# Performance work log

Hardware: AMD Instinct MI355X
Metric: run time of the kernel (lower is better)

## Reference

```python
import jax, jax.numpy as jnp
import numpy as np

D_MODEL = 512
N_HEADS = 8
D_FF = 2048

def _linear_params(key, d_in, d_out):
    kw, kb = jax.random.split(key)
    bound = 1.0 / np.sqrt(d_in)
    W = jax.random.uniform(kw, (d_in, d_out), minval=-bound, maxval=bound, dtype=jnp.float32)
    b = jax.random.uniform(kb, (d_out,), minval=-bound, maxval=bound, dtype=jnp.float32)
    return W, b

def setup_inputs() -> dict:
    key = jax.random.key(0)
    ks = jax.random.split(key, 7)
    x = jax.random.normal(ks[0], (4, 2048, D_MODEL), dtype=jnp.float32)
    Wq, bq = _linear_params(ks[1], D_MODEL, D_MODEL)
    Wk, bk = _linear_params(ks[2], D_MODEL, D_MODEL)
    Wv, bv = _linear_params(ks[3], D_MODEL, D_MODEL)
    W1, b1 = _linear_params(ks[4], D_MODEL, D_FF)
    W2, b2 = _linear_params(ks[5], D_FF, D_MODEL)
    g1 = jnp.ones((D_MODEL,), jnp.float32); be1 = jnp.zeros((D_MODEL,), jnp.float32)
    g2 = jnp.ones((D_MODEL,), jnp.float32); be2 = jnp.zeros((D_MODEL,), jnp.float32)
    return {"x": x, "Wq": Wq, "bq": bq, "Wk": Wk, "bk": bk, "Wv": Wv, "bv": bv,
            "W1": W1, "b1": b1, "W2": W2, "b2": b2,
            "g1": g1, "be1": be1, "g2": g2, "be2": be2}

def _layernorm(x, g, b, eps=1e-5):
    mu = jnp.mean(x, axis=-1, keepdims=True)
    var = jnp.mean(jnp.square(x - mu), axis=-1, keepdims=True)
    return (x - mu) * jax.lax.rsqrt(var + eps) * g + b

def reference(x, Wq, bq, Wk, bk, Wv, bv, W1, b1, W2, b2, g1, be1, g2, be2):
    B, S, D = x.shape
    H = N_HEADS
    Dh = D // H
    residual = x
    xn = _layernorm(x, g1, be1)
    # [B,S,D] -> [B,H,S,Dh]
    q = (xn @ Wq + bq).reshape(B, S, H, Dh).transpose(0, 2, 1, 3)
    k = (xn @ Wk + bk).reshape(B, S, H, Dh).transpose(0, 2, 1, 3)
    v = (xn @ Wv + bv).reshape(B, S, H, Dh).transpose(0, 2, 1, 3)
    # sigmoid pointwise attention, scaled by sqrt(d_model) (not head dim)
    scores = jnp.einsum('bhsd,bhtd->bhst', q, k) / jnp.sqrt(jnp.float32(D))
    attn = jax.nn.sigmoid(scores)
    out = jnp.einsum('bhst,bhtd->bhsd', attn, v)
    out = out.transpose(0, 2, 1, 3).reshape(B, S, D)
    x = residual + out  # dropout=0 (eval)
    residual = x
    xn = _layernorm(x, g2, be2)
    ffn = jax.nn.relu(xn @ W1 + b1) @ W2 + b2
    return residual + ffn
```

## Files before the change

kernel.cpp:

```cpp
#include <hip/hip_runtime.h>
#include <hip/hip_bf16.h>
#include <math.h>

#define D_MODEL 512
#define N_HEADS 8
#define D_HEAD 64
#define D_FF 2048
#define SEQ 2048
#define BATCH 4
#define NTOK (BATCH * SEQ)
#define QSCALE 0.04419417382415922f
#define QSCALE_L2E (-QSCALE * 1.44269504089f)

typedef unsigned short ushort_t;
typedef __attribute__((ext_vector_type(8))) short short8;
typedef __attribute__((ext_vector_type(4))) short short4v;
typedef __attribute__((ext_vector_type(4))) float float4v;

static __device__ __forceinline__ ushort_t f2bf(float f) {
    union { float f; unsigned int i; } c; c.f = f;
    unsigned int i = c.i;
    unsigned int r = (i + 0x7FFFu + ((i >> 16) & 1u)) >> 16;
    return (ushort_t)r;
}

static __device__ __forceinline__ unsigned int pack2bf(float a, float b) {
    union { __hip_bfloat162 h; unsigned int u; } c;
    c.h = __float22bfloat162_rn(make_float2(a, b));
    return c.u;
}

static __device__ __forceinline__ float sig2(float x) {
    return __builtin_amdgcn_rcpf(1.0f + __builtin_amdgcn_exp2f(x));
}

__global__ __launch_bounds__(256) void k_prep_weights(const float* __restrict__ Wq,
                                                      const float* __restrict__ Wk,
                                                      const float* __restrict__ Wv,
                                                      const float* __restrict__ W1,
                                                      const float* __restrict__ W2,
                                                      ushort_t* __restrict__ Wqkvt,
                                                      ushort_t* __restrict__ W1t,
                                                      ushort_t* __restrict__ W2t) {
    __shared__ ushort_t tile[64][66];
    int bid = blockIdx.x;
    const float* src; ushort_t* dst; int K, N, tk, tn;
    if (bid < 192) {
        int m = bid >> 6, r = bid & 63;
        src = (m == 0) ? Wq : ((m == 1) ? Wk : Wv);
        dst = Wqkvt + (size_t)m * 512 * 512; K = 512; N = 512; tk = r >> 3; tn = r & 7;
    } else if (bid < 448) {
        int r = bid - 192; src = W1; dst = W1t; K = 512; N = 2048; tk = r >> 5; tn = r & 31;
    } else {
        int r = bid - 448; src = W2; dst = W2t; K = 2048; N = 512; tk = r >> 3; tn = r & 7;
    }
    int k0 = tk * 64, n0 = tn * 64;
    int rr = threadIdx.x >> 6, c = threadIdx.x & 63;
#pragma unroll
    for (int i = 0; i < 16; i++) {
        int row = i * 4 + rr;
        tile[row][c] = f2bf(src[(size_t)(k0 + row) * N + n0 + c]);
    }
    __syncthreads();
#pragma unroll
    for (int i = 0; i < 16; i++) {
        int row = i * 4 + rr;
        dst[(size_t)(n0 + row) * K + k0 + c] = tile[c][row];
    }
}

__global__ __launch_bounds__(256) void k_layernorm(const float* __restrict__ X,
                                                   const float* __restrict__ g,
                                                   const float* __restrict__ be,
                                                   ushort_t* __restrict__ Out) {
    int row  = blockIdx.x * 4 + (threadIdx.x >> 6);
    int lane = threadIdx.x & 63;
    const float* x = X + (size_t)row * D_MODEL + lane * 8;
    float4 v0 = ((const float4*)x)[0];
    float4 v1 = ((const float4*)x)[1];
    float vals[8] = {v0.x, v0.y, v0.z, v0.w, v1.x, v1.y, v1.z, v1.w};
    float s = 0.f, sq = 0.f;
#pragma unroll
    for (int j = 0; j < 8; j++) { s += vals[j]; sq += vals[j] * vals[j]; }
#pragma unroll
    for (int off = 32; off; off >>= 1) { s += __shfl_xor(s, off); sq += __shfl_xor(sq, off); }
    float mu  = s * (1.0f / D_MODEL);
    float var = sq * (1.0f / D_MODEL) - mu * mu;
    float inv = rsqrtf(var + 1e-5f);
    const float* gp  = g  + lane * 8;
    const float* bp  = be + lane * 8;
    float4 g0 = ((const float4*)gp)[0], g1v = ((const float4*)gp)[1];
    float4 b0 = ((const float4*)bp)[0], b1v = ((const float4*)bp)[1];
    float gs[8] = {g0.x, g0.y, g0.z, g0.w, g1v.x, g1v.y, g1v.z, g1v.w};
    float bs[8] = {b0.x, b0.y, b0.z, b0.w, b1v.x, b1v.y, b1v.z, b1v.w};
    ushort_t o[8];
#pragma unroll
    for (int j = 0; j < 8; j++) o[j] = f2bf((vals[j] - mu) * inv * gs[j] + bs[j]);
    ushort_t* op = Out + (size_t)row * D_MODEL + lane * 8;
    *(uint4*)op = *(uint4*)o;
}

static __device__ __forceinline__ void stage_tile(const ushort_t* __restrict__ G, int K,
                                                  ushort_t* L, int nchunks, int koff,
                                                  int w, int l) {
#pragma unroll
    for (int n = w; n < nchunks; n += 4) {
        const ushort_t* g = G + (size_t)(n * 16 + (l >> 2)) * K + koff + (l & 3) * 8;
        __builtin_amdgcn_global_load_lds((const __attribute__((address_space(1))) void*)g,
                                         (__attribute__((address_space(3))) void*)(L + n * 512),
                                         16, 0, 0);
    }
}

template <int JW>
static __device__ __forceinline__ void gemm_core2(const ushort_t* __restrict__ A,
                                                  const ushort_t* __restrict__ Bt,
                                                  int K, int m0, int n0,
                                                  ushort_t* As, ushort_t* Bs,
                                                  float4v acc[4][JW]) {
    const int BBUF = JW * 1024;
    int t = threadIdx.x, w = t >> 6, l = t & 63, q = l >> 4, lm = l & 15;
    int mb = (w & 1) * 64, nb = (w >> 1) * (JW * 16);
    const ushort_t* Ab = A + (size_t)m0 * K;
    const ushort_t* Bb = Bt + (size_t)n0 * K;
    int T = K >> 5;

    stage_tile(Ab, K, As, 8, 0, w, l);
    stage_tile(Bb, K, Bs, 2 * JW, 0, w, l);
    __syncthreads();

    for (int kt = 0; kt < T; kt++) {
        int cur = kt & 1;
        if (kt + 1 < T) {
            stage_tile(Ab, K, As + (1 - cur) * 4096, 8, (kt + 1) * 32, w, l);
            stage_tile(Bb, K, Bs + (1 - cur) * BBUF, 2 * JW, (kt + 1) * 32, w, l);
        }
        const ushort_t* asb = As + cur * 4096;
        const ushort_t* bsb = Bs + cur * BBUF;
        short8 a[4], b[JW];
#pragma unroll
        for (int i = 0; i < 4; i++) a[i] = *(const short8*)&asb[(mb + 16 * i + lm) * 32 + q * 8];
#pragma unroll
        for (int j = 0; j < JW; j++) b[j] = *(const short8*)&bsb[(nb + 16 * j + lm) * 32 + q * 8];
#pragma unroll
        for (int i = 0; i < 4; i++)
#pragma unroll
            for (int j = 0; j < JW; j++)
                acc[i][j] = __builtin_amdgcn_mfma_f32_16x16x32_bf16(a[i], b[j], acc[i][j], 0, 0, 0);
        __syncthreads();
    }
}

__global__ __launch_bounds__(256) void k_gemm_qkv(const ushort_t* __restrict__ A,
                                                  const ushort_t* __restrict__ Bt,
                                                  const float* __restrict__ bq,
                                                  const float* __restrict__ bk,
                                                  const float* __restrict__ bv,
                                                  ushort_t* __restrict__ qb,
                                                  ushort_t* __restrict__ kb,
                                                  ushort_t* __restrict__ vt) {
    __shared__ __align__(16) ushort_t As[8192];
    __shared__ __align__(16) ushort_t Bs[8192];
    int m0 = blockIdx.x * 128, n0 = blockIdx.y * 128;
    float4v acc[4][4];
#pragma unroll
    for (int i = 0; i < 4; i++)
#pragma unroll
        for (int j = 0; j < 4; j++) acc[i][j] = (float4v){0.f, 0.f, 0.f, 0.f};
    gemm_core2<4>(A, Bt, D_MODEL, m0, n0, As, Bs, acc);

    int t = threadIdx.x, w = t >> 6, l = t & 63, q = l >> 4, lm = l & 15;
    int mb = (w & 1) * 64, nb = (w >> 1) * 64;
    int mat = n0 >> 9, c0 = n0 & 511;
    const float* bias = (mat == 0) ? bq : ((mat == 1) ? bk : bv);
#pragma unroll
    for (int j = 0; j < 4; j++) {
        int cl = c0 + nb + 16 * j + lm;
        int hh = cl >> 6, dh = cl & 63;
        float bvv = bias[cl];
#pragma unroll
        for (int i = 0; i < 4; i++) {
            int mr0 = m0 + mb + 16 * i + q * 4;
            int bb = mr0 >> 11, ss0 = mr0 & (SEQ - 1);
            if (mat == 2) {
                union { ushort_t s[4]; uint2 v; } pk;
#pragma unroll
                for (int r = 0; r < 4; r++) pk.s[r] = f2bf(acc[i][j][r] + bvv);
                *(uint2*)&vt[((size_t)(bb * N_HEADS + hh) * D_HEAD + dh) * SEQ + ss0] = pk.v;
            } else {
                ushort_t* dst = (mat == 0) ? qb : kb;
                float sc = (mat == 0) ? QSCALE_L2E : 1.0f;
#pragma unroll
                for (int r = 0; r < 4; r++)
                    dst[((size_t)(bb * N_HEADS + hh) * SEQ + ss0 + r) * D_HEAD + dh] =
                        f2bf((acc[i][j][r] + bvv) * sc);
            }
        }
    }
}

__global__ __launch_bounds__(256) void k_gemm_ffn1(const ushort_t* __restrict__ A,
                                                   const ushort_t* __restrict__ Bt,
                                                   const float* __restrict__ b1,
                                                   ushort_t* __restrict__ hb) {
    __shared__ __align__(16) ushort_t As[8192];
    __shared__ __align__(16) ushort_t Bs[8192];
    int m0 = blockIdx.x * 128, n0 = blockIdx.y * 128;
    float4v acc[4][4];
#pragma unroll
    for (int i = 0; i < 4; i++)
#pragma unroll
        for (int j = 0; j < 4; j++) acc[i][j] = (float4v){0.f, 0.f, 0.f, 0.f};
    gemm_core2<4>(A, Bt, D_MODEL, m0, n0, As, Bs, acc);

    int t = threadIdx.x, w = t >> 6, l = t & 63, q = l >> 4, lm = l & 15;
    int mb = (w & 1) * 64, nb = (w >> 1) * 64;
#pragma unroll
    for (int j = 0; j < 4; j++) {
        int cl = n0 + nb + 16 * j + lm;
        float bvv = b1[cl];
#pragma unroll
        for (int i = 0; i < 4; i++) {
            int mr0 = m0 + mb + 16 * i + q * 4;
#pragma unroll
            for (int r = 0; r < 4; r++)
                hb[(size_t)(mr0 + r) * D_FF + cl] = f2bf(fmaxf(acc[i][j][r] + bvv, 0.f));
        }
    }
}

__global__ __launch_bounds__(256) void k_gemm_ffn2(const ushort_t* __restrict__ A,
                                                   const ushort_t* __restrict__ Bt,
                                                   const float* __restrict__ b2,
                                                   const float* __restrict__ res,
                                                   float* __restrict__ out) {
    __shared__ __align__(16) ushort_t As[8192];
    __shared__ __align__(16) ushort_t Bs[4096];
    int m0 = blockIdx.x * 128, n0 = blockIdx.y * 64;
    float4v acc[4][2];
#pragma unroll
    for (int i = 0; i < 4; i++)
#pragma unroll
        for (int j = 0; j < 2; j++) acc[i][j] = (float4v){0.f, 0.f, 0.f, 0.f};
    gemm_core2<2>(A, Bt, D_FF, m0, n0, As, Bs, acc);

    int t = threadIdx.x, w = t >> 6, l = t & 63, q = l >> 4, lm = l & 15;
    int mb = (w & 1) * 64, nb = (w >> 1) * 32;
#pragma unroll
    for (int j = 0; j < 2; j++) {
        int cl = n0 + nb + 16 * j + lm;
        float bvv = b2[cl];
#pragma unroll
        for (int i = 0; i < 4; i++) {
            int mr0 = m0 + mb + 16 * i + q * 4;
#pragma unroll
            for (int r = 0; r < 4; r++) {
                size_t idx = (size_t)(mr0 + r) * D_MODEL + cl;
                out[idx] = acc[i][j][r] + bvv + res[idx];
            }
        }
    }
}

static __device__ __forceinline__ void qkt_step(const ushort_t* __restrict__ ksb, int koff,
                                                const short8 qf[2][2], float4v st[2]) {
    short8 kf0 = *(const short8*)&ksb[koff];
    short8 kf1 = *(const short8*)&ksb[koff + 32];
    st[0] = (float4v){0.f, 0.f, 0.f, 0.f};
    st[1] = (float4v){0.f, 0.f, 0.f, 0.f};
#pragma unroll
    for (int nt = 0; nt < 2; nt++) {
        st[nt] = __builtin_amdgcn_mfma_f32_16x16x32_bf16(kf0, qf[nt][0], st[nt], 0, 0, 0);
        st[nt] = __builtin_amdgcn_mfma_f32_16x16x32_bf16(kf1, qf[nt][1], st[nt], 0, 0, 0);
    }
}

static __device__ __forceinline__ void sig_pv(const ushort_t* __restrict__ vsb, int voff,
                                              const float4v st[2], float4v o[2][4]) {
    short4v pf[2];
#pragma unroll
    for (int nt = 0; nt < 2; nt++) {
        union { unsigned int u[2]; short4v v; } pk;
        pk.u[0] = pack2bf(sig2(st[nt][0]), sig2(st[nt][1]));
        pk.u[1] = pack2bf(sig2(st[nt][2]), sig2(st[nt][3]));
        pf[nt] = pk.v;
    }
#pragma unroll
    for (int dj = 0; dj < 4; dj++) {
        short4v vf = *(const short4v*)&vsb[dj * 16 * 136 + voff];
#pragma unroll
        for (int nt = 0; nt < 2; nt++)
            o[nt][dj] = __builtin_amdgcn_mfma_f32_16x16x16bf16_1k(vf, pf[nt], o[nt][dj], 0, 0, 0);
    }
}

__global__ __launch_bounds__(512, 4) void k_attention(const ushort_t* __restrict__ Q,
                                                      const ushort_t* __restrict__ Kb,
                                                      const ushort_t* __restrict__ Vt,
                                                      const float* __restrict__ X,
                                                      float* __restrict__ Y) {
    __shared__ __align__(16) char smem[71680];
    ushort_t* Ks = (ushort_t*)smem;
    ushort_t* Vs = (ushort_t*)(smem + 36864);
    float*  Osum = (float*)smem;

    const int KBUF = 128 * 72;
    const int VBUF = 64 * 136;
    const int NIT  = SEQ / 128;

    int bh = blockIdx.y;
    int b = bh >> 3, h = bh & 7;
    size_t base = (size_t)bh * SEQ * D_HEAD;
    int s0 = blockIdx.x * 128;
    int t = threadIdx.x, w = t >> 6, l = t & 63, q = l >> 4, lm = l & 15;
    int g = w >> 1, th = w & 1;
    int srow = t >> 3, sc = (t & 7) * 8;
    int srowV = t >> 4, scV = (t & 15) * 8;

    short8 qf[2][2];
#pragma unroll
    for (int nt = 0; nt < 2; nt++)
#pragma unroll
        for (int kc = 0; kc < 2; kc++) {
            const ushort_t* qg = Q + base + (size_t)(s0 + 32 * g + 16 * nt + lm) * D_HEAD + kc * 32 + q * 8;
            uint4 u = *(const uint4*)qg;
            qf[nt][kc] = *(const short8*)&u;
        }

    float4v o[2][4];
#pragma unroll
    for (int nt = 0; nt < 2; nt++)
#pragma unroll
        for (int dj = 0; dj < 4; dj++) o[nt][dj] = (float4v){0.f, 0.f, 0.f, 0.f};

    const ushort_t* kg0 = Kb + base + (size_t)srow * D_HEAD + sc;
    const ushort_t* vg0 = Vt + base + (size_t)srowV * SEQ + scV;

    uint4 kr0, kr1, vr0, vr1;
    kr0 = *(const uint4*)(kg0);
    kr1 = *(const uint4*)(kg0 + 64 * D_HEAD);
    vr0 = *(const uint4*)(vg0);
    vr1 = *(const uint4*)(vg0 + 32 * SEQ);
    *(uint4*)&Ks[srow * 72 + sc]          = kr0;
    *(uint4*)&Ks[(srow + 64) * 72 + sc]   = kr1;
    *(uint4*)&Vs[srowV * 136 + scV]       = vr0;
    *(uint4*)&Vs[(srowV + 32) * 136 + scV] = vr1;
    kr0 = *(const uint4*)(kg0 + 128 * D_HEAD);
    kr1 = *(const uint4*)(kg0 + 192 * D_HEAD);
    vr0 = *(const uint4*)(vg0 + 128);
    vr1 = *(const uint4*)(vg0 + 32 * SEQ + 128);
    __syncthreads();

    int kbase = (64 * th + lm) * 72 + q * 8;
    int vbase = lm * 136 + 64 * th + 4 * q;

    for (int tt = 0; tt < NIT; tt++) {
        int cur = tt & 1;
        const ushort_t* ksb = Ks + cur * KBUF;
        const ushort_t* vsb = Vs + cur * VBUF;

        if (tt + 1 < NIT) {
            int nxt = 1 - cur;
            *(uint4*)&Ks[nxt * KBUF + srow * 72 + sc]           = kr0;
            *(uint4*)&Ks[nxt * KBUF + (srow + 64) * 72 + sc]    = kr1;
            *(uint4*)&Vs[nxt * VBUF + srowV * 136 + scV]        = vr0;
            *(uint4*)&Vs[nxt * VBUF + (srowV + 32) * 136 + scV] = vr1;
            if (tt + 2 < NIT) {
                size_t ko = (size_t)(tt + 2) * 128 * D_HEAD;
                size_t vo = (size_t)(tt + 2) * 128;
                kr0 = *(const uint4*)(kg0 + ko);
                kr1 = *(const uint4*)(kg0 + ko + 64 * D_HEAD);
                vr0 = *(const uint4*)(vg0 + vo);
                vr1 = *(const uint4*)(vg0 + vo + 32 * SEQ);
            }
        }

        float4v st[2][2];
        qkt_step(ksb, kbase, qf, st[0]);
#pragma unroll
        for (int mt = 1; mt < 4; mt++) {
            qkt_step(ksb, kbase + 16 * 72 * mt, qf, st[mt & 1]);
            sig_pv(vsb, vbase + 16 * (mt - 1), st[(mt - 1) & 1], o);
        }
        sig_pv(vsb, vbase + 48, st[1], o);

        __syncthreads();
    }

    if (th == 0) {
#pragma unroll
        for (int nt = 0; nt < 2; nt++)
#pragma unroll
            for (int dj = 0; dj < 4; dj++) {
                float4v v = o[nt][dj];
                *(float4*)&Osum[(32 * g + 16 * nt + lm) * 68 + 16 * dj + 4 * q] =
                    make_float4(v[0], v[1], v[2], v[3]);
            }
    }
    __syncthreads();
    if (th == 1) {
#pragma unroll
        for (int nt = 0; nt < 2; nt++)
#pragma unroll
            for (int dj = 0; dj < 4; dj++) {
                float* p = &Osum[(32 * g + 16 * nt + lm) * 68 + 16 * dj + 4 * q];
                float4 old = *(float4*)p;
                float4v v = o[nt][dj];
                *(float4*)p = make_float4(old.x + v[0], old.y + v[1], old.z + v[2], old.w + v[3]);
            }
    }
    __syncthreads();

    {
        int row = t >> 2, c0 = (t & 3) * 16;
        size_t gro = ((size_t)(b * SEQ + s0 + row)) * D_MODEL + h * D_HEAD + c0;
        const float* xp = X + gro;
        float* yp = Y + gro;
        const float* os = &Osum[row * 68 + c0];
#pragma unroll
        for (int i = 0; i < 4; i++) {
            float4 xv = *(const float4*)(xp + i * 4);
            float4 ov = *(const float4*)(os + i * 4);
            float4 rr;
            rr.x = xv.x + ov.x; rr.y = xv.y + ov.y;
            rr.z = xv.z + ov.z; rr.w = xv.w + ov.w;
            *(float4*)(yp + i * 4) = rr;
        }
    }
}

extern "C" void kernel_launch(void* const* d_in, const int* in_sizes, int n_in,
                              void* d_out, int out_size, void* d_ws, size_t ws_size,
                              hipStream_t stream) {
    const float* x   = (const float*)d_in[0];
    const float* Wq  = (const float*)d_in[1];
    const float* bq  = (const float*)d_in[2];
    const float* Wk  = (const float*)d_in[3];
    const float* bk  = (const float*)d_in[4];
    const float* Wv  = (const float*)d_in[5];
    const float* bv  = (const float*)d_in[6];
    const float* W1  = (const float*)d_in[7];
    const float* b1  = (const float*)d_in[8];
    const float* W2  = (const float*)d_in[9];
    const float* b2  = (const float*)d_in[10];
    const float* g1  = (const float*)d_in[11];
    const float* be1 = (const float*)d_in[12];
    const float* g2  = (const float*)d_in[13];
    const float* be2 = (const float*)d_in[14];
    float* out = (float*)d_out;

    char* p = (char*)d_ws;
    ushort_t* xn    = (ushort_t*)p; p += (size_t)NTOK * D_MODEL * 2;
    ushort_t* yn    = (ushort_t*)p; p += (size_t)NTOK * D_MODEL * 2;
    float*    y     = (float*)p;    p += (size_t)NTOK * D_MODEL * 4;
    ushort_t* qb    = (ushort_t*)p; p += (size_t)NTOK * D_MODEL * 2;
    ushort_t* kb    = (ushort_t*)p; p += (size_t)NTOK * D_MODEL * 2;
    ushort_t* vt    = (ushort_t*)p; p += (size_t)NTOK * D_MODEL * 2;
    ushort_t* hb    = (ushort_t*)p; p += (size_t)NTOK * D_FF * 2;
    ushort_t* Wqkvt = (ushort_t*)p; p += (size_t)3 * D_MODEL * D_MODEL * 2;
    ushort_t* W1t   = (ushort_t*)p; p += (size_t)D_MODEL * D_FF * 2;
    ushort_t* W2t   = (ushort_t*)p; p += (size_t)D_FF * D_MODEL * 2;

    k_prep_weights<<<704, 256, 0, stream>>>(Wq, Wk, Wv, W1, W2, Wqkvt, W1t, W2t);

    k_layernorm<<<NTOK / 4, 256, 0, stream>>>(x, g1, be1, xn);

    dim3 gq(NTOK / 128, (3 * D_MODEL) / 128);
    k_gemm_qkv<<<gq, 256, 0, stream>>>(xn, Wqkvt, bq, bk, bv, qb, kb, vt);

    dim3 ga(SEQ / 128, BATCH * N_HEADS);
    k_attention<<<ga, 512, 0, stream>>>(qb, kb, vt, x, y);

    k_layernorm<<<NTOK / 4, 256, 0, stream>>>(y, g2, be2, yn);

    dim3 g1d(NTOK / 128, D_FF / 128);
    k_gemm_ffn1<<<g1d, 256, 0, stream>>>(yn, W1t, b1, hb);
    dim3 g2d(NTOK / 128, D_MODEL / 64);
    k_gemm_ffn2<<<g2d, 256, 0, stream>>>(hb, W2t, b2, y, out);
}
```

Measured before the change: 245.8 us.

## Load K/V attention fragments directly from global memory instead of LDS staging

Removes the double-buffered LDS staging of K and V tiles in the attention kernel, along with its register prefetch and per-iteration barrier. Each wave now reads its MFMA operand fragments straight from global memory, relying on the L1/L2 caches for reuse across the waves of a block. This drops the LDS traffic and barrier cost and frees shared memory, which could allow more blocks per CU. The cost is that each K/V tile is fetched from global memory once per wave group rather than once per block, and the explicit prefetch that hid load latency is gone.

```diff
diff --git a/kernel.cpp b/kernel.cpp
--- a/kernel.cpp
+++ b/kernel.cpp
@@ -262,51 +262,14 @@
     }
 }
 
-static __device__ __forceinline__ void qkt_step(const ushort_t* __restrict__ ksb, int koff,
-                                                const short8 qf[2][2], float4v st[2]) {
-    short8 kf0 = *(const short8*)&ksb[koff];
-    short8 kf1 = *(const short8*)&ksb[koff + 32];
-    st[0] = (float4v){0.f, 0.f, 0.f, 0.f};
-    st[1] = (float4v){0.f, 0.f, 0.f, 0.f};
-#pragma unroll
-    for (int nt = 0; nt < 2; nt++) {
-        st[nt] = __builtin_amdgcn_mfma_f32_16x16x32_bf16(kf0, qf[nt][0], st[nt], 0, 0, 0);
-        st[nt] = __builtin_amdgcn_mfma_f32_16x16x32_bf16(kf1, qf[nt][1], st[nt], 0, 0, 0);
-    }
-}
-
-static __device__ __forceinline__ void sig_pv(const ushort_t* __restrict__ vsb, int voff,
-                                              const float4v st[2], float4v o[2][4]) {
-    short4v pf[2];
-#pragma unroll
-    for (int nt = 0; nt < 2; nt++) {
-        union { unsigned int u[2]; short4v v; } pk;
-        pk.u[0] = pack2bf(sig2(st[nt][0]), sig2(st[nt][1]));
-        pk.u[1] = pack2bf(sig2(st[nt][2]), sig2(st[nt][3]));
-        pf[nt] = pk.v;
-    }
-#pragma unroll
-    for (int dj = 0; dj < 4; dj++) {
-        short4v vf = *(const short4v*)&vsb[dj * 16 * 136 + voff];
-#pragma unroll
-        for (int nt = 0; nt < 2; nt++)
-            o[nt][dj] = __builtin_amdgcn_mfma_f32_16x16x16bf16_1k(vf, pf[nt], o[nt][dj], 0, 0, 0);
-    }
-}
-
 __global__ __launch_bounds__(512, 4) void k_attention(const ushort_t* __restrict__ Q,
                                                       const ushort_t* __restrict__ Kb,
                                                       const ushort_t* __restrict__ Vt,
                                                       const float* __restrict__ X,
                                                       float* __restrict__ Y) {
-    __shared__ __align__(16) char smem[71680];
-    ushort_t* Ks = (ushort_t*)smem;
-    ushort_t* Vs = (ushort_t*)(smem + 36864);
-    float*  Osum = (float*)smem;
-
-    const int KBUF = 128 * 72;
-    const int VBUF = 64 * 136;
-    const int NIT  = SEQ / 128;
+    __shared__ __align__(16) float Osum[128 * 68];
+
+    const int NIT = SEQ / 128;
 
     int bh = blockIdx.y;
     int b = bh >> 3, h = bh & 7;
@@ -314,8 +277,6 @@
     int s0 = blockIdx.x * 128;
     int t = threadIdx.x, w = t >> 6, l = t & 63, q = l >> 4, lm = l & 15;
     int g = w >> 1, th = w & 1;
-    int srow = t >> 3, sc = (t & 7) * 8;
-    int srowV = t >> 4, scV = (t & 15) * 8;
 
     short8 qf[2][2];
 #pragma unroll
@@ -333,58 +294,46 @@
 #pragma unroll
         for (int dj = 0; dj < 4; dj++) o[nt][dj] = (float4v){0.f, 0.f, 0.f, 0.f};
 
-    const ushort_t* kg0 = Kb + base + (size_t)srow * D_HEAD + sc;
-    const ushort_t* vg0 = Vt + base + (size_t)srowV * SEQ + scV;
-
-    uint4 kr0, kr1, vr0, vr1;
-    kr0 = *(const uint4*)(kg0);
-    kr1 = *(const uint4*)(kg0 + 64 * D_HEAD);
-    vr0 = *(const uint4*)(vg0);
-    vr1 = *(const uint4*)(vg0 + 32 * SEQ);
-    *(uint4*)&Ks[srow * 72 + sc]          = kr0;
-    *(uint4*)&Ks[(srow + 64) * 72 + sc]   = kr1;
-    *(uint4*)&Vs[srowV * 136 + scV]       = vr0;
-    *(uint4*)&Vs[(srowV + 32) * 136 + scV] = vr1;
-    kr0 = *(const uint4*)(kg0 + 128 * D_HEAD);
-    kr1 = *(const uint4*)(kg0 + 192 * D_HEAD);
-    vr0 = *(const uint4*)(vg0 + 128);
-    vr1 = *(const uint4*)(vg0 + 32 * SEQ + 128);
-    __syncthreads();
-
-    int kbase = (64 * th + lm) * 72 + q * 8;
-    int vbase = lm * 136 + 64 * th + 4 * q;
+    const ushort_t* kgw = Kb + base + (size_t)(64 * th + lm) * D_HEAD + q * 8;
+    const ushort_t* vgw = Vt + base + (size_t)lm * SEQ + 64 * th + 4 * q;
 
     for (int tt = 0; tt < NIT; tt++) {
-        int cur = tt & 1;
-        const ushort_t* ksb = Ks + cur * KBUF;
-        const ushort_t* vsb = Vs + cur * VBUF;
-
-        if (tt + 1 < NIT) {
-            int nxt = 1 - cur;
-            *(uint4*)&Ks[nxt * KBUF + srow * 72 + sc]           = kr0;
-            *(uint4*)&Ks[nxt * KBUF + (srow + 64) * 72 + sc]    = kr1;
-            *(uint4*)&Vs[nxt * VBUF + srowV * 136 + scV]        = vr0;
-            *(uint4*)&Vs[nxt * VBUF + (srowV + 32) * 136 + scV] = vr1;
-            if (tt + 2 < NIT) {
-                size_t ko = (size_t)(tt + 2) * 128 * D_HEAD;
-                size_t vo = (size_t)(tt + 2) * 128;
-                kr0 = *(const uint4*)(kg0 + ko);
-                kr1 = *(const uint4*)(kg0 + ko + 64 * D_HEAD);
-                vr0 = *(const uint4*)(vg0 + vo);
-                vr1 = *(const uint4*)(vg0 + vo + 32 * SEQ);
-            }
-        }
-
-        float4v st[2][2];
-        qkt_step(ksb, kbase, qf, st[0]);
-#pragma unroll
-        for (int mt = 1; mt < 4; mt++) {
-            qkt_step(ksb, kbase + 16 * 72 * mt, qf, st[mt & 1]);
-            sig_pv(vsb, vbase + 16 * (mt - 1), st[(mt - 1) & 1], o);
-        }
-        sig_pv(vsb, vbase + 48, st[1], o);
-
-        __syncthreads();
+        const ushort_t* kp = kgw + (size_t)tt * 128 * D_HEAD;
+        const ushort_t* vp = vgw + tt * 128;
+
+#pragma unroll
+        for (int mt = 0; mt < 4; mt++) {
+            short8 kf0, kf1;
+            {
+                uint4 u0 = *(const uint4*)(kp + (size_t)(16 * mt) * D_HEAD);
+                uint4 u1 = *(const uint4*)(kp + (size_t)(16 * mt) * D_HEAD + 32);
+                kf0 = *(const short8*)&u0;
+                kf1 = *(const short8*)&u1;
+            }
+            float4v st[2];
+            st[0] = (float4v){0.f, 0.f, 0.f, 0.f};
+            st[1] = (float4v){0.f, 0.f, 0.f, 0.f};
+#pragma unroll
+            for (int nt = 0; nt < 2; nt++) {
+                st[nt] = __builtin_amdgcn_mfma_f32_16x16x32_bf16(kf0, qf[nt][0], st[nt], 0, 0, 0);
+                st[nt] = __builtin_amdgcn_mfma_f32_16x16x32_bf16(kf1, qf[nt][1], st[nt], 0, 0, 0);
+            }
+            short4v pf[2];
+#pragma unroll
+            for (int nt = 0; nt < 2; nt++) {
+                union { unsigned int u[2]; short4v v; } pk;
+                pk.u[0] = pack2bf(sig2(st[nt][0]), sig2(st[nt][1]));
+                pk.u[1] = pack2bf(sig2(st[nt][2]), sig2(st[nt][3]));
+                pf[nt] = pk.v;
+            }
+#pragma unroll
+            for (int dj = 0; dj < 4; dj++) {
+                short4v vf = *(const short4v*)(vp + (size_t)(16 * dj) * SEQ + 16 * mt);
+#pragma unroll
+                for (int nt = 0; nt < 2; nt++)
+                    o[nt][dj] = __builtin_amdgcn_mfma_f32_16x16x16bf16_1k(vf, pf[nt], o[nt][dj], 0, 0, 0);
+            }
+        }
     }
 
     if (th == 0) {
```

Measured after the change: 364.9 us. 1.48x slower.
